# Performance work log

Measured on AMD Instinct MI355X. Metric: run time of the kernel, lower is better.

The kernel has to match this reference:

```python
import jax, jax.numpy as jnp
import numpy as np

B = 4096
HASH_BITS = 128
TEACHER_DIM = 768
TEMPERATURE = 0.2
CONTRASTIVE_W = 1.0
DISTILL_W = 0.5
QUANT_W = 0.01


def _l2_normalize(x, eps=1e-12):
    # matches torch F.normalize(dim=-1)
    n = jnp.sqrt(jnp.sum(x * x, axis=-1, keepdims=True))
    return x / jnp.maximum(n, eps)


def setup_inputs() -> dict:
    key = jax.random.key(0)
    k1, k2, k3, k4 = jax.random.split(key, 4)
    logits = jax.random.normal(k1, (B, HASH_BITS), dtype=jnp.float32)
    # binary {-1,+1} codes as in the module contract
    hash_codes = jnp.sign(jax.random.normal(k2, (B, HASH_BITS), dtype=jnp.float32))
    hash_codes = jnp.where(hash_codes == 0, 1.0, hash_codes)
    teacher_embed = jax.random.normal(k3, (B, TEACHER_DIM), dtype=jnp.float32)
    # sparse random positives plus self-positives (guarantees each row nonempty)
    rand_pos = jax.random.uniform(k4, (B, B)) < 0.002
    eye = jnp.eye(B, dtype=bool)
    positive_mask = rand_pos | eye
    return {
        "logits": logits,
        "hash_codes": hash_codes,
        "teacher_embed": teacher_embed,
        "positive_mask": positive_mask,
    }


def reference(logits, hash_codes, teacher_embed, positive_mask):
    teacher = _l2_normalize(teacher_embed)

    # ---- contrastive (vectorized form of the per-row python loop) ----
    ln = _l2_normalize(logits)
    sim = (ln @ ln.T) / TEMPERATURE  # [B, B]
    eye = jnp.eye(sim.shape[0], dtype=bool)
    sim_masked = jnp.where(eye, -jnp.inf, sim)
    # per-row stable logsumexp over self-masked similarities
    log_denom = jax.nn.logsumexp(sim_masked, axis=1)  # [B]
    pm = positive_mask.astype(sim.dtype)
    cnt = pm.sum(axis=1)  # [B]
    pos_mean = (sim * pm).sum(axis=1) / jnp.maximum(cnt, 1.0)
    has_pos = cnt > 0
    per_row = jnp.where(has_pos, -pos_mean + log_denom, 0.0)
    num_pos = jnp.maximum(has_pos.sum(), 1)
    loss_cont = per_row.sum() / num_pos.astype(sim.dtype)

    # ---- distillation: hash similarity vs teacher similarity MSE ----
    hash_sim = (hash_codes @ hash_codes.T) / hash_codes.shape[-1]
    teacher_sim = teacher @ teacher.T
    loss_distill = jnp.mean((hash_sim - teacher_sim) ** 2)

    # ---- quantization: push |logits| toward 1 ----
    loss_quant = jnp.mean(jnp.abs(jnp.abs(logits) - 1.0))

    total = (
        CONTRASTIVE_W * loss_cont
        + DISTILL_W * loss_distill
        + QUANT_W * loss_quant
    )
    return total
```

## Files before the change

kernel.cpp:

```cpp
#include <hip/hip_runtime.h>


typedef __bf16 bf16x8 __attribute__((ext_vector_type(8)));
typedef float f32x4 __attribute__((ext_vector_type(4)));

__device__ __forceinline__ unsigned short f2bf(float f) {
  union { float f; unsigned int u; } v; v.f = f;
  unsigned int u = v.u;
  return (unsigned short)((u + 0x7FFFu + ((u >> 16) & 1u)) >> 16);
}

__global__ __launch_bounds__(256) void prep(const float* __restrict__ logits,
                                            const float* __restrict__ hash,
                                            const float* __restrict__ teacher,
                                            unsigned short* __restrict__ P,
                                            unsigned char* __restrict__ QT,
                                            float* __restrict__ qpart,
                                            float* __restrict__ rowexp,
                                            float* __restrict__ possum,
                                            float* __restrict__ cntw,
                                            float* __restrict__ dtot) {
  __shared__ float rnt[16];
  __shared__ unsigned char QL[16 * 897];
  const int t = threadIdx.x, wave = t >> 6, lane = t & 63;
  const int r0 = (int)blockIdx.x * 16;

#pragma unroll
  for (int rr = 0; rr < 4; ++rr) {
    const int rl = wave * 4 + rr, r = r0 + rl;
    float ss = 0.f;
#pragma unroll
    for (int i = 0; i < 12; ++i) {
      const float v = teacher[(size_t)r * 768 + i * 64 + lane];
      ss += v * v;
    }
    const float l0 = logits[(size_t)r * 128 + lane];
    const float l1 = logits[(size_t)r * 128 + 64 + lane];
    float ssl = l0 * l0 + l1 * l1;
    float qv = fabsf(fabsf(l0) - 1.f) + fabsf(fabsf(l1) - 1.f);
#pragma unroll
    for (int off = 1; off < 64; off <<= 1) {
      ss += __shfl_xor(ss, off, 64);
      ssl += __shfl_xor(ssl, off, 64);
      qv += __shfl_xor(qv, off, 64);
    }
    const float rnl = 1.f / fmaxf(sqrtf(ssl), 1e-12f);
    P[(size_t)r * 128 + lane] = f2bf(l0 * rnl);
    P[(size_t)r * 128 + 64 + lane] = f2bf(l1 * rnl);
    if (lane == 0) {
      rnt[rl] = 11.313708498984761f / fmaxf(sqrtf(ss), 1e-12f);
      qpart[r] = qv;
    }
  }
  if (t < 16) { rowexp[r0 + t] = 0.f; possum[r0 + t] = 0.f; cntw[r0 + t] = 0.f; }
  if (blockIdx.x == 0 && t == 0) *dtot = 0.f;
  __syncthreads();

#pragma unroll
  for (int it = 0; it < 4; ++it) {
    const int task = it * 256 + t;
    if (task < 896) {
      const int r = task / 56, cb = task % 56;
      const int r_g = r0 + r;
      unsigned char* dst = &QL[r * 897 + cb * 16];
      if (cb < 8) {
        const float4 v0 = *(const float4*)&hash[(size_t)r_g * 128 + cb * 16];
        const float4 v1 = *(const float4*)&hash[(size_t)r_g * 128 + cb * 16 + 4];
        const float4 v2 = *(const float4*)&hash[(size_t)r_g * 128 + cb * 16 + 8];
        const float4 v3 = *(const float4*)&hash[(size_t)r_g * 128 + cb * 16 + 12];
        const float vv[16] = {v0.x, v0.y, v0.z, v0.w, v1.x, v1.y, v1.z, v1.w,
                              v2.x, v2.y, v2.z, v2.w, v3.x, v3.y, v3.z, v3.w};
#pragma unroll
        for (int k = 0; k < 16; ++k) dst[k] = vv[k] >= 0.f ? 0x38 : 0xB8;
      } else {
        const float sc = rnt[r];
        const int c0 = cb * 16 - 128;
        const float4 v0 = *(const float4*)&teacher[(size_t)r_g * 768 + c0];
        const float4 v1 = *(const float4*)&teacher[(size_t)r_g * 768 + c0 + 4];
        const float4 v2 = *(const float4*)&teacher[(size_t)r_g * 768 + c0 + 8];
        const float4 v3 = *(const float4*)&teacher[(size_t)r_g * 768 + c0 + 12];
        const float vv[16] = {v0.x, v0.y, v0.z, v0.w, v1.x, v1.y, v1.z, v1.w,
                              v2.x, v2.y, v2.z, v2.w, v3.x, v3.y, v3.z, v3.w};
#pragma unroll
        for (int k = 0; k < 16; ++k) {
          const int p8 = __builtin_amdgcn_cvt_pk_fp8_f32(vv[k] * sc, vv[k] * sc,
                                                         0, false);
          dst[k] = (unsigned char)(p8 & 0xFF);
        }
      }
    }
  }
  __syncthreads();

#pragma unroll
  for (int i = 0; i < 4; ++i) {
    const int c = t + 256 * i;
    if (c < 896) {
      unsigned char buf[16];
#pragma unroll
      for (int j = 0; j < 16; ++j) buf[j] = QL[j * 897 + c];
      *(uint4*)&QT[(size_t)c * 4096 + r0] = *(uint4*)buf;
    }
  }
}

#define STAGE_GEN(GA, GB, PITCH)                                               \
  {                                                                            \
    _Pragma("unroll") for (int it = 0; it < 4; ++it) {                         \
      const int task = it * 256 + t;                                           \
      const int row = task >> 3;                                               \
      const int c16 = (task & 7) ^ (row & 7);                                  \
      const unsigned char* gpA = (GA) + (size_t)row * (PITCH) + c16 * 16;      \
      __builtin_amdgcn_global_load_lds(                                        \
          (const __attribute__((address_space(1))) void*)gpA,                  \
          (__attribute__((address_space(3))) void*)&SB[it * 4096 + wave * 1024],\
          16, 0, 0);                                                           \
      if (offdiag) {                                                           \
        const unsigned char* gpB = (GB) + (size_t)row * (PITCH) + c16 * 16;    \
        __builtin_amdgcn_global_load_lds(                                      \
            (const __attribute__((address_space(1))) void*)gpB,                \
            (__attribute__((address_space(3)))                                 \
                 void*)&SB[16384 + it * 4096 + wave * 1024],                   \
            16, 0, 0);                                                         \
      }                                                                        \
    }                                                                          \
  }

#define MFMA_B()                                                               \
  {                                                                            \
    _Pragma("unroll") for (int ks = 0; ks < 2; ++ks) {                         \
      const int ph = ((ks * 4 + qd) ^ (l15 & 7)) * 16;                         \
      bf16x8 af[4], bfr[4];                                                    \
      _Pragma("unroll") for (int rt = 0; rt < 4; ++rt)                         \
          af[rt] = *(const bf16x8*)&SB[(wy * 64 + rt * 16 + l15) * 128 + ph];  \
      _Pragma("unroll") for (int ct = 0; ct < 4; ++ct)                         \
          bfr[ct] = *(const bf16x8*)&SB[boffB +                                \
                                        (wx * 64 + ct * 16 + l15) * 128 + ph]; \
      _Pragma("unroll") for (int rt = 0; rt < 4; ++rt)                         \
          _Pragma("unroll") for (int ct = 0; ct < 4; ++ct) acc[rt][ct] =       \
          __builtin_amdgcn_mfma_f32_16x16x32_bf16(af[rt], bfr[ct],             \
                                                  acc[rt][ct], 0, 0, 0);       \
    }                                                                          \
  }

#define MFMA_Q()                                                               \
  {                                                                            \
    _Pragma("unroll") for (int ks = 0; ks < 4; ++ks) {                         \
      const int g0 = ks * 4 + qd;                                              \
      const int ph = ((g0 >> 1) ^ (l15 & 7)) * 16 + (g0 & 1) * 8;              \
      long af[4], bfr[4];                                                      \
      _Pragma("unroll") for (int rt = 0; rt < 4; ++rt)                         \
          af[rt] = *(const long*)&SB[(wy * 64 + rt * 16 + l15) * 128 + ph];    \
      _Pragma("unroll") for (int ct = 0; ct < 4; ++ct)                         \
          bfr[ct] = *(const long*)&SB[boffB +                                  \
                                      (wx * 64 + ct * 16 + l15) * 128 + ph];   \
      _Pragma("unroll") for (int rt = 0; rt < 4; ++rt)                         \
          _Pragma("unroll") for (int ct = 0; ct < 4; ++ct) acc[rt][ct] =       \
          __builtin_amdgcn_mfma_f32_16x16x32_fp8_fp8(af[rt], bfr[ct],          \
                                                     acc[rt][ct], 0, 0, 0);    \
    }                                                                          \
  }

__global__ __launch_bounds__(256, 3) void mega(const unsigned short* __restrict__ P,
                                               const unsigned char* __restrict__ QT,
                                               const void* __restrict__ mask,
                                               float* __restrict__ rowexp,
                                               float* __restrict__ possum,
                                               float* __restrict__ cntw,
                                               float* __restrict__ dtot) {
  __shared__ __align__(16) unsigned char SB[32768];
  __shared__ float redrow[128][2], red4[4];

  const int t = threadIdx.x;
  const int wave = t >> 6, lane = t & 63;
  const int qd = lane >> 4, l15 = lane & 15;
  const int wy = wave >> 1, wx = wave & 1;
  const int b = (int)blockIdx.x;

  f32x4 acc[4][4];
#pragma unroll
  for (int rt = 0; rt < 4; ++rt)
#pragma unroll
    for (int ct = 0; ct < 4; ++ct) acc[rt][ct] = {0.f, 0.f, 0.f, 0.f};

  if (b < 28) {
    int I = 0, rem = b;
    while (rem >= 7 - I) { rem -= 7 - I; ++I; }
    const int J = I + rem;
    const bool offdiag = (I != J);
    const int boffB = offdiag ? 16384 : 0;
    const unsigned char* QA = QT + (size_t)I * 128 * 4096;
    const unsigned char* QB = QT + (size_t)J * 128 * 4096;
    for (int kc = 0; kc < 32; ++kc) {
      __syncthreads();
      STAGE_GEN(QA + kc * 128, QB + kc * 128, 4096);
      __syncthreads();
      MFMA_Q();
    }
    float dsum = 0.f;
#pragma unroll
    for (int rt = 0; rt < 4; ++rt)
#pragma unroll
      for (int ct = 0; ct < 4; ++ct)
#pragma unroll
        for (int i = 0; i < 4; ++i) dsum += acc[rt][ct][i] * acc[rt][ct][i];
#pragma unroll
    for (int off = 1; off < 64; off <<= 1) dsum += __shfl_xor(dsum, off, 64);
    if (lane == 0) red4[wave] = dsum;
    __syncthreads();
    if (t == 0) {
      const float mult = (I == J ? 1.f : 2.f) *
                         (((I == 0) == (J == 0)) ? 1.f : -1.f);
      atomicAdd(dtot, mult * (red4[0] + red4[1] + red4[2] + red4[3]));
    }
  } else {
    const int bb = b - 28;
    const int l = (bb & 7) * 128 + (bb >> 3);
    const int bi = l >> 5, bj = l & 31;
    const int ti = bi * 128, tj = bj * 128;
    const bool offdiag = (bi != bj);
    const int boffB = offdiag ? 16384 : 0;

    const unsigned char* Pa = (const unsigned char*)(P + (size_t)ti * 128);
    const unsigned char* Pb = (const unsigned char*)(P + (size_t)tj * 128);
    for (int kc = 0; kc < 2; ++kc) {
      __syncthreads();
      STAGE_GEN(Pa + kc * 128, Pb + kc * 128, 256);
      __syncthreads();
      MFMA_B();
    }

    __syncthreads();
    unsigned char* MD = SB;
    const bool is_byte = ((const unsigned char*)mask)[4097] != 0;
    if (is_byte) {
      const unsigned char* m8d = (const unsigned char*)mask + (size_t)ti * 4096 + tj;
#pragma unroll
      for (int it = 0; it < 4; ++it) {
        const int task = it * 256 + t;
        const int row = task >> 3, seg = task & 7;
        __builtin_amdgcn_global_load_lds(
            (const __attribute__((address_space(1))) void*)
                (m8d + (size_t)row * 4096 + seg * 16),
            (__attribute__((address_space(3))) void*)&MD[it * 4096 + wave * 1024],
            16, 0, 0);
      }
    } else {
      const unsigned int* m32 = (const unsigned int*)mask;
#pragma unroll
      for (int it = 0; it < 16; ++it) {
        const int task = it * 256 + t;
        const int row = task >> 5, seg = task & 31;
        const uint4 v = *(const uint4*)&m32[(size_t)(ti + row) * 4096 + tj + seg * 4];
        uchar4 pk;
        pk.x = v.x ? 1 : 0; pk.y = v.y ? 1 : 0;
        pk.z = v.z ? 1 : 0; pk.w = v.w ? 1 : 0;
        *(uchar4*)&MD[row * 128 + seg * 4] = pk;
      }
    }
    __syncthreads();

#pragma unroll
    for (int rt = 0; rt < 4; ++rt) {
#pragma unroll
      for (int r = 0; r < 4; ++r) {
        const int mrow = wy * 64 + rt * 16 + qd * 4 + r;
        const int m = ti + mrow;
        float se = 0.f;
#pragma unroll
        for (int ct = 0; ct < 4; ++ct) {
          const int ncol = wx * 64 + ct * 16 + l15;
          const int n = tj + ncol;
          const float sim = acc[rt][ct][r] * 5.0f;
          const float e = __expf(sim);
          if (m != n) se += e;
          if (MD[mrow * 128 + ncol]) {
            atomicAdd(&possum[m], sim);
            atomicAdd(&cntw[m], 1.0f);
          }
        }
#pragma unroll
        for (int off = 1; off < 16; off <<= 1) se += __shfl_xor(se, off, 64);
        if (l15 == 0) redrow[mrow][wx] = se;
      }
    }
    __syncthreads();
    if (t < 128) atomicAdd(&rowexp[ti + t], redrow[t][0] + redrow[t][1]);
  }
}

__global__ __launch_bounds__(1024) void finalize(const float* __restrict__ rowexp,
                                                 const float* __restrict__ possum,
                                                 const float* __restrict__ cnt,
                                                 const float* __restrict__ qpart,
                                                 const float* __restrict__ dtot,
                                                 float* __restrict__ out) {
  const int t = threadIdx.x;
  const int wave = t >> 6, lane = t & 63;
  float c = 0.f, q = 0.f;
  for (int m = t; m < 4096; m += 1024) {
    c += logf(rowexp[m]) - possum[m] / fmaxf(cnt[m], 1.0f);
    q += qpart[m];
  }
#pragma unroll
  for (int off = 1; off < 64; off <<= 1) {
    c += __shfl_xor(c, off, 64);
    q += __shfl_xor(q, off, 64);
  }
  __shared__ float sc[16], sq[16];
  if (lane == 0) { sc[wave] = c; sq[wave] = q; }
  __syncthreads();
  if (t == 0) {
    float C = 0.f, Q = 0.f;
    for (int i = 0; i < 16; ++i) { C += sc[i]; Q += sq[i]; }
    out[0] = C * (1.0f / 4096.0f) + 0.5f * (dtot[0] * 3.6379788e-12f) +
             0.01f * (Q * (1.0f / 524288.0f));
  }
}

extern "C" void kernel_launch(void* const* d_in, const int* in_sizes, int n_in,
                              void* d_out, int out_size, void* d_ws, size_t ws_size,
                              hipStream_t stream) {
  const float* logits = (const float*)d_in[0];
  const float* hash = (const float*)d_in[1];
  const float* teacher = (const float*)d_in[2];
  const void* mask = d_in[3];
  float* out = (float*)d_out;

  char* ws = (char*)d_ws;
  float* rowexp = (float*)(ws + 0);
  float* possum = (float*)(ws + 16384);
  float* cntw = (float*)(ws + 32768);
  float* qpart = (float*)(ws + 49152);
  float* dtot = (float*)(ws + 65536);
  unsigned short* P = (unsigned short*)(ws + 98304);
  unsigned char* QT = (unsigned char*)(ws + 98304 + 1048576);

  prep<<<256, 256, 0, stream>>>(logits, hash, teacher, P, QT, qpart, rowexp,
                                possum, cntw, dtot);
  mega<<<1052, 256, 0, stream>>>(P, QT, mask, rowexp, possum, cntw, dtot);
  finalize<<<1, 1024, 0, stream>>>(rowexp, possum, cntw, qpart, dtot, out);
}
```

Measured before the change: 156.3 us.

## Split-K the distillation Gram tiles, atomically accumulate, and prefetch mask earlier

The 28 distillation Gram-tile blocks, each running 32 K-chunks, become 224 blocks each handling 4 chunks. They atomically add partial results into an 896x896 fp32 buffer that prep zeroes, and a new gsq kernel reduces the squared entries with sign and symmetry weights. This is meant to remove the long-tail imbalance where 28 heavy blocks dominate the mega kernel. The contrastive blocks now issue the byte-mask async LDS load into a dedicated buffer before the bf16 MFMA, overlapping it with compute, and prep vectorizes its loads and stores. The cost is many float atomics, an extra kernel launch, more LDS per block, and sums that depend on atomic ordering.

```diff
diff --git a/kernel.cpp b/kernel.cpp
--- a/kernel.cpp
+++ b/kernel.cpp
@@ -19,25 +19,28 @@
                                             float* __restrict__ rowexp,
                                             float* __restrict__ possum,
                                             float* __restrict__ cntw,
-                                            float* __restrict__ dtot) {
+                                            float* __restrict__ dtot,
+                                            float* __restrict__ Cbuf) {
   __shared__ float rnt[16];
   __shared__ unsigned char QL[16 * 897];
   const int t = threadIdx.x, wave = t >> 6, lane = t & 63;
   const int r0 = (int)blockIdx.x * 16;
 
+  for (int i = t; i < 784; i += 256)
+    *(f32x4*)&Cbuf[((size_t)blockIdx.x * 784 + i) * 4] = (f32x4){0.f, 0.f, 0.f, 0.f};
+
 #pragma unroll
   for (int rr = 0; rr < 4; ++rr) {
     const int rl = wave * 4 + rr, r = r0 + rl;
     float ss = 0.f;
 #pragma unroll
-    for (int i = 0; i < 12; ++i) {
-      const float v = teacher[(size_t)r * 768 + i * 64 + lane];
-      ss += v * v;
-    }
-    const float l0 = logits[(size_t)r * 128 + lane];
-    const float l1 = logits[(size_t)r * 128 + 64 + lane];
-    float ssl = l0 * l0 + l1 * l1;
-    float qv = fabsf(fabsf(l0) - 1.f) + fabsf(fabsf(l1) - 1.f);
+    for (int i = 0; i < 3; ++i) {
+      const float4 v = *(const float4*)&teacher[(size_t)r * 768 + i * 256 + lane * 4];
+      ss += v.x * v.x + v.y * v.y + v.z * v.z + v.w * v.w;
+    }
+    const float2 lv = *(const float2*)&logits[(size_t)r * 128 + lane * 2];
+    float ssl = lv.x * lv.x + lv.y * lv.y;
+    float qv = fabsf(fabsf(lv.x) - 1.f) + fabsf(fabsf(lv.y) - 1.f);
 #pragma unroll
     for (int off = 1; off < 64; off <<= 1) {
       ss += __shfl_xor(ss, off, 64);
@@ -45,8 +48,9 @@
       qv += __shfl_xor(qv, off, 64);
     }
     const float rnl = 1.f / fmaxf(sqrtf(ssl), 1e-12f);
-    P[(size_t)r * 128 + lane] = f2bf(l0 * rnl);
-    P[(size_t)r * 128 + 64 + lane] = f2bf(l1 * rnl);
+    const unsigned int pk = (unsigned int)f2bf(lv.x * rnl) |
+                            ((unsigned int)f2bf(lv.y * rnl) << 16);
+    *(unsigned int*)&P[(size_t)r * 128 + lane * 2] = pk;
     if (lane == 0) {
       rnt[rl] = 11.313708498984761f / fmaxf(sqrtf(ss), 1e-12f);
       qpart[r] = qv;
@@ -167,9 +171,10 @@
                                                float* __restrict__ rowexp,
                                                float* __restrict__ possum,
                                                float* __restrict__ cntw,
-                                               float* __restrict__ dtot) {
+                                               float* __restrict__ Cbuf) {
   __shared__ __align__(16) unsigned char SB[32768];
-  __shared__ float redrow[128][2], red4[4];
+  __shared__ __align__(16) unsigned char MD[16384];
+  __shared__ float redrow[128][2];
 
   const int t = threadIdx.x;
   const int wave = t >> 6, lane = t & 63;
@@ -183,55 +188,41 @@
 #pragma unroll
     for (int ct = 0; ct < 4; ++ct) acc[rt][ct] = {0.f, 0.f, 0.f, 0.f};
 
-  if (b < 28) {
-    int I = 0, rem = b;
+  if (b < 224) {
+    const int tile = b % 28, ks = b / 28;
+    int I = 0, rem = tile;
     while (rem >= 7 - I) { rem -= 7 - I; ++I; }
     const int J = I + rem;
     const bool offdiag = (I != J);
     const int boffB = offdiag ? 16384 : 0;
-    const unsigned char* QA = QT + (size_t)I * 128 * 4096;
-    const unsigned char* QB = QT + (size_t)J * 128 * 4096;
-    for (int kc = 0; kc < 32; ++kc) {
+    const unsigned char* QA = QT + (size_t)I * 128 * 4096 + ks * 512;
+    const unsigned char* QB = QT + (size_t)J * 128 * 4096 + ks * 512;
+    for (int kc = 0; kc < 4; ++kc) {
       __syncthreads();
       STAGE_GEN(QA + kc * 128, QB + kc * 128, 4096);
       __syncthreads();
       MFMA_Q();
     }
-    float dsum = 0.f;
-#pragma unroll
-    for (int rt = 0; rt < 4; ++rt)
-#pragma unroll
-      for (int ct = 0; ct < 4; ++ct)
-#pragma unroll
-        for (int i = 0; i < 4; ++i) dsum += acc[rt][ct][i] * acc[rt][ct][i];
-#pragma unroll
-    for (int off = 1; off < 64; off <<= 1) dsum += __shfl_xor(dsum, off, 64);
-    if (lane == 0) red4[wave] = dsum;
-    __syncthreads();
-    if (t == 0) {
-      const float mult = (I == J ? 1.f : 2.f) *
-                         (((I == 0) == (J == 0)) ? 1.f : -1.f);
-      atomicAdd(dtot, mult * (red4[0] + red4[1] + red4[2] + red4[3]));
+    float* Ct = Cbuf + (size_t)I * 128 * 896 + J * 128;
+#pragma unroll
+    for (int rt = 0; rt < 4; ++rt) {
+      const int row = wy * 64 + rt * 16 + qd * 4;
+#pragma unroll
+      for (int ct = 0; ct < 4; ++ct) {
+        const int col = wx * 64 + ct * 16 + l15;
+#pragma unroll
+        for (int i = 0; i < 4; ++i)
+          atomicAdd(&Ct[(size_t)(row + i) * 896 + col], acc[rt][ct][i]);
+      }
     }
   } else {
-    const int bb = b - 28;
+    const int bb = b - 224;
     const int l = (bb & 7) * 128 + (bb >> 3);
     const int bi = l >> 5, bj = l & 31;
     const int ti = bi * 128, tj = bj * 128;
     const bool offdiag = (bi != bj);
     const int boffB = offdiag ? 16384 : 0;
 
-    const unsigned char* Pa = (const unsigned char*)(P + (size_t)ti * 128);
-    const unsigned char* Pb = (const unsigned char*)(P + (size_t)tj * 128);
-    for (int kc = 0; kc < 2; ++kc) {
-      __syncthreads();
-      STAGE_GEN(Pa + kc * 128, Pb + kc * 128, 256);
-      __syncthreads();
-      MFMA_B();
-    }
-
-    __syncthreads();
-    unsigned char* MD = SB;
     const bool is_byte = ((const unsigned char*)mask)[4097] != 0;
     if (is_byte) {
       const unsigned char* m8d = (const unsigned char*)mask + (size_t)ti * 4096 + tj;
@@ -245,7 +236,19 @@
             (__attribute__((address_space(3))) void*)&MD[it * 4096 + wave * 1024],
             16, 0, 0);
       }
-    } else {
+    }
+
+    const unsigned char* Pa = (const unsigned char*)(P + (size_t)ti * 128);
+    const unsigned char* Pb = (const unsigned char*)(P + (size_t)tj * 128);
+    for (int kc = 0; kc < 2; ++kc) {
+      __syncthreads();
+      STAGE_GEN(Pa + kc * 128, Pb + kc * 128, 256);
+      __syncthreads();
+      MFMA_B();
+    }
+
+    __syncthreads();
+    if (!is_byte) {
       const unsigned int* m32 = (const unsigned int*)mask;
 #pragma unroll
       for (int it = 0; it < 16; ++it) {
@@ -257,8 +260,8 @@
         pk.z = v.z ? 1 : 0; pk.w = v.w ? 1 : 0;
         *(uchar4*)&MD[row * 128 + seg * 4] = pk;
       }
-    }
-    __syncthreads();
+      __syncthreads();
+    }
 
 #pragma unroll
     for (int rt = 0; rt < 4; ++rt) {
@@ -287,6 +290,32 @@
     __syncthreads();
     if (t < 128) atomicAdd(&rowexp[ti + t], redrow[t][0] + redrow[t][1]);
   }
+}
+
+__global__ __launch_bounds__(256) void gsq(const float* __restrict__ C,
+                                           float* __restrict__ dtot) {
+  const int t = threadIdx.x;
+  const int wave = t >> 6, lane = t & 63;
+  float s = 0.f;
+  for (int q = (int)blockIdx.x * 256 + t; q < 200704; q += 256 * 256) {
+    const f32x4 v = *(const f32x4*)&C[(size_t)q * 4];
+    const int r = q / 224;
+    const int c0 = (q - r * 224) * 4;
+    const int Ir = r >> 7;
+#pragma unroll
+    for (int k = 0; k < 4; ++k) {
+      const int Jc = (c0 + k) >> 7;
+      const float w = (Ir == Jc) ? 1.f : 2.f;
+      const float sg = ((Ir == 0) == (Jc == 0)) ? w : -w;
+      s += sg * v[k] * v[k];
+    }
+  }
+#pragma unroll
+  for (int off = 1; off < 64; off <<= 1) s += __shfl_xor(s, off, 64);
+  __shared__ float sw[4];
+  if (lane == 0) sw[wave] = s;
+  __syncthreads();
+  if (t == 0) atomicAdd(dtot, sw[0] + sw[1] + sw[2] + sw[3]);
 }
 
 __global__ __launch_bounds__(1024) void finalize(const float* __restrict__ rowexp,
@@ -335,9 +364,11 @@
   float* dtot = (float*)(ws + 65536);
   unsigned short* P = (unsigned short*)(ws + 98304);
   unsigned char* QT = (unsigned char*)(ws + 98304 + 1048576);
+  float* Cbuf = (float*)(ws + 98304 + 1048576 + 3670016);
 
   prep<<<256, 256, 0, stream>>>(logits, hash, teacher, P, QT, qpart, rowexp,
-                                possum, cntw, dtot);
-  mega<<<1052, 256, 0, stream>>>(P, QT, mask, rowexp, possum, cntw, dtot);
+                                possum, cntw, dtot, Cbuf);
+  mega<<<1248, 256, 0, stream>>>(P, QT, mask, rowexp, possum, cntw, Cbuf);
+  gsq<<<256, 256, 0, stream>>>(Cbuf, dtot);
   finalize<<<1, 1024, 0, stream>>>(rowexp, possum, cntw, qpart, dtot, out);
 }
```

New measurement: 153.4 us. No clear change (-1.8%).
